# Optimization experiments

Hardware: AMD Instinct MI355X
Metric: run time of the kernel (lower is better)

Reference implementation:

```python
import jax, jax.numpy as jnp
import numpy as np
from jax.scipy.special import erf

B, S, D = 8, 512, 512
H = 8            # num_heads per half
DH = D // 2      # 256, per-branch model dim
DFF = 2048
HOUT = 2


def _layernorm(x, g, b, eps=1e-6):
    mu = jnp.mean(x, axis=-1, keepdims=True)
    var = jnp.mean(jnp.square(x - mu), axis=-1, keepdims=True)
    return (x - mu) / jnp.sqrt(var + eps) * g + b


def _rescale_dist(w):
    one = jnp.float32(1.0)
    return (one + jnp.exp(one)) / (one + jnp.exp(one - w))


def _mha(xin, wq, bq, wk, bk, wv, bv, wo, bo, maskf, adjoin, dist):
    b, s, dm = xin.shape
    dep = dm // H
    def heads(t):
        return t.reshape(b, s, H, dep).transpose(0, 2, 1, 3)  # (b,h,s,dep)
    q = heads(xin @ wq + bq)
    k = heads(xin @ wk + bk)
    v = heads(xin @ wv + bv)
    scores = jnp.einsum('bhqd,bhkd->bhqk', q, k)
    scale = jnp.sqrt(jnp.float32(dep))
    if dist is not None:
        scores = jax.nn.relu(scores) * _rescale_dist(dist) / scale
    else:
        scores = scores / scale
    scores = scores + maskf * jnp.float32(-1e9)
    if adjoin is not None:
        scores = scores + adjoin
    attn = jax.nn.softmax(scores, axis=-1)
    out = jnp.einsum('bhqk,bhkd->bhqd', attn, v).transpose(0, 2, 1, 3).reshape(b, s, dm)
    return out @ wo + bo, attn


def setup_inputs() -> dict:
    key = jax.random.key(0)
    ks = jax.random.split(key, 32)
    init = lambda k, shp: (jax.random.normal(k, shp, dtype=jnp.float32) * 0.02)
    inp = {
        'x': jax.random.normal(ks[0], (B, S, D), dtype=jnp.float32),
        'adjoin_matrix': jax.random.normal(ks[1], (B, 1, S, S), dtype=jnp.float32),
        'dist_matrix': jax.random.uniform(ks[2], (B, 1, S, S), dtype=jnp.float32),
        # mha1 (adjoin branch)
        'wq1': init(ks[3], (DH, DH)), 'bq1': jnp.zeros((DH,), jnp.float32),
        'wk1': init(ks[4], (DH, DH)), 'bk1': jnp.zeros((DH,), jnp.float32),
        'wv1': init(ks[5], (DH, DH)), 'bv1': jnp.zeros((DH,), jnp.float32),
        'wo1': init(ks[6], (DH, DH)), 'bo1': jnp.zeros((DH,), jnp.float32),
        # mha2 (distance branch)
        'wq2': init(ks[7], (DH, DH)), 'bq2': jnp.zeros((DH,), jnp.float32),
        'wk2': init(ks[8], (DH, DH)), 'bk2': jnp.zeros((DH,), jnp.float32),
        'wv2': init(ks[9], (DH, DH)), 'bv2': jnp.zeros((DH,), jnp.float32),
        'wo2': init(ks[10], (DH, DH)), 'bo2': jnp.zeros((DH,), jnp.float32),
        # BANLayer
        'vnet_w': init(ks[11], (DH, 2 * DH)), 'vnet_b': jnp.zeros((2 * DH,), jnp.float32),
        'qnet_w': init(ks[12], (DH, 2 * DH)), 'qnet_b': jnp.zeros((2 * DH,), jnp.float32),
        'h_mat': init(ks[13], (1, HOUT, 1, 2 * DH)),
        'h_bias': init(ks[14], (1, HOUT, 1, 1)),
        'bn_gamma': jnp.ones((D,), jnp.float32), 'bn_beta': jnp.zeros((D,), jnp.float32),
        'bn_mean': jnp.zeros((D,), jnp.float32), 'bn_var': jnp.ones((D,), jnp.float32),
        # LayerNorms
        'ln1_g': jnp.ones((D,), jnp.float32), 'ln1_b': jnp.zeros((D,), jnp.float32),
        'ln2_g': jnp.ones((D,), jnp.float32), 'ln2_b': jnp.zeros((D,), jnp.float32),
        # FFN
        'ffn_w1': init(ks[15], (D, DFF)), 'ffn_b1': jnp.zeros((DFF,), jnp.float32),
        'ffn_w2': init(ks[16], (DFF, D)), 'ffn_b2': jnp.zeros((D,), jnp.float32),
        # padding mask (int -> cast), 1 = masked
        'encoder_padding_mask': jax.random.randint(ks[17], (B, 1, 1, S), 0, 2, dtype=jnp.int32),
    }
    return inp


def reference(x, adjoin_matrix, dist_matrix,
              wq1, bq1, wk1, bk1, wv1, bv1, wo1, bo1,
              wq2, bq2, wk2, bk2, wv2, bv2, wo2, bo2,
              vnet_w, vnet_b, qnet_w, qnet_b, h_mat, h_bias,
              bn_gamma, bn_beta, bn_mean, bn_var,
              ln1_g, ln1_b, ln2_g, ln2_b,
              ffn_w1, ffn_b1, ffn_w2, ffn_b2,
              encoder_padding_mask):
    maskf = encoder_padding_mask.astype(jnp.float32)
    x1, x2 = jnp.split(x, 2, axis=-1)
    # local branch: adjoin bias, no distance
    x_l, aw_local = _mha(x1, wq1, bq1, wk1, bk1, wv1, bv1, wo1, bo1, maskf, adjoin_matrix, None)
    # global branch: relu + distance rescale, no adjoin
    x_g, aw_global = _mha(x2, wq2, bq2, wk2, bk2, wv2, bv2, wo2, bo2, maskf, None, dist_matrix)
    # BANLayer (h_out=2 <= c, eval mode; p_net is identity for rows=1)
    v_ = jax.nn.relu(x_l @ vnet_w + vnet_b)   # (B,S,2*DH)
    q_ = jax.nn.relu(x_g @ qnet_w + qnet_b)
    att_maps = jnp.einsum('xhyk,bvk,bqk->bhvq', h_mat, v_, q_) + h_bias  # (B,HOUT,S,S)
    logits = jnp.einsum('bvk,bhvq,bqk->bvk', v_, att_maps, q_)           # sum over h
    logits = (logits - bn_mean) / jnp.sqrt(bn_var + 1e-3) * bn_gamma + bn_beta
    attn_output = logits * jnp.concatenate([x_l, x_g], axis=-1)
    out1 = _layernorm(x + attn_output, ln1_g, ln1_b)
    h = out1 @ ffn_w1 + ffn_b1
    h = 0.5 * h * (1.0 + erf(h / jnp.sqrt(jnp.float32(2.0))))  # exact gelu
    ffn_out = h @ ffn_w2 + ffn_b2
    out2 = _layernorm(out1 + ffn_out, ln2_g, ln2_b)
    return (out2, aw_local, aw_global)
```

## Files before the change

### kernel.cpp

```cpp
#include <hip/hip_runtime.h>
#include <hip/hip_bf16.h>

typedef __hip_bfloat16 bf16;
typedef __attribute__((ext_vector_type(8))) short bf16x8;
typedef __attribute__((ext_vector_type(4))) float f32x4;

#define BB 8
#define SS 512
#define DD 512
#define NH 8
#define DHm 256
#define DFF 2048

__device__ __forceinline__ void gl_lds16(const void* g, void* l) {
  __builtin_amdgcn_global_load_lds((const __attribute__((address_space(1))) void*)g,
                                   (__attribute__((address_space(3))) void*)l, 16, 0, 0);
}

__device__ __forceinline__ bf16x8 cvt8(const float* p) {
  union { bf16x8 v; bf16 h[8]; } u;
  float4 f0 = *(const float4*)p, f1 = *(const float4*)(p + 4);
  u.h[0]=__float2bfloat16(f0.x); u.h[1]=__float2bfloat16(f0.y);
  u.h[2]=__float2bfloat16(f0.z); u.h[3]=__float2bfloat16(f0.w);
  u.h[4]=__float2bfloat16(f1.x); u.h[5]=__float2bfloat16(f1.y);
  u.h[6]=__float2bfloat16(f1.z); u.h[7]=__float2bfloat16(f1.w);
  return u.v;
}

template<int BM, int BN, int SMODE, int BIASM, int ACT>
__global__ __launch_bounds__(256)
void gemm2(const bf16* __restrict__ A, const bf16* __restrict__ B,
           const float* __restrict__ bias, float* __restrict__ Cf,
           bf16* __restrict__ Cb, int K, int lda, int ldb, int ldc,
           long long sA, long long sB, long long sC)
{
  __shared__ bf16 As[BM * 32];
  __shared__ bf16 Bs[BN * 32];
  const int t = threadIdx.x, lane = t & 63, wave = t >> 6;
  const int l15 = lane & 15, quad = lane >> 4;
  constexpr int WMT = BM / 32, WNT = BN / 32;
  const int wm = (wave & 1) * (BM / 2), wn = (wave >> 1) * (BN / 2);
  const int row0 = blockIdx.y * BM, col0 = blockIdx.x * BN;
  const bf16* Ab = A + (long long)blockIdx.z * sA + (long long)row0 * lda;
  const bf16* Bb = B + (long long)blockIdx.z * sB + (long long)col0 * ldb;
  const int srow = wave * 16 + (lane >> 2), skc = (lane & 3) << 3;

  f32x4 acc[WMT][WNT] = {};

  for (int k0 = 0; k0 < K; k0 += 32) {
#pragma unroll
    for (int j = 0; j < BM / 64; j++)
      gl_lds16(Ab + (long long)(srow + j * 64) * lda + k0 + skc,
               (char*)As + wave * 1024 + j * 4096);
#pragma unroll
    for (int j = 0; j < BN / 64; j++)
      gl_lds16(Bb + (long long)(srow + j * 64) * ldb + k0 + skc,
               (char*)Bs + wave * 1024 + j * 4096);
    __syncthreads();
    bf16x8 af[WMT], bfr[WNT];
#pragma unroll
    for (int i = 0; i < WMT; i++) af[i]  = *(const bf16x8*)&As[(wm + i * 16 + l15) * 32 + quad * 8];
#pragma unroll
    for (int j = 0; j < WNT; j++) bfr[j] = *(const bf16x8*)&Bs[(wn + j * 16 + l15) * 32 + quad * 8];
#pragma unroll
    for (int i = 0; i < WMT; i++)
#pragma unroll
      for (int j = 0; j < WNT; j++)
        acc[i][j] = __builtin_amdgcn_mfma_f32_16x16x32_bf16(af[i], bfr[j], acc[i][j], 0, 0, 0);
    __syncthreads();
  }

  float sb = 0.f;
  if (BIASM == 2) sb = bias[0] + bias[1];
#pragma unroll
  for (int i = 0; i < WMT; i++)
#pragma unroll
    for (int j = 0; j < WNT; j++) {
      int col = col0 + wn + j * 16 + l15;
      float bv = (BIASM == 1) ? bias[col] : sb;
#pragma unroll
      for (int r = 0; r < 4; r++) {
        int row = row0 + wm + i * 16 + (quad << 2) + r;
        float v = acc[i][j][r] + bv;
        if (ACT == 1) v = fmaxf(v, 0.f);
        if (ACT == 2) v = 0.5f * v * (1.f + erff(v * 0.70710678118654752f));
        long long ci = (long long)blockIdx.z * sC + (long long)row * ldc + col;
        if (SMODE & 1) Cf[ci] = v;
        if (SMODE & 2) Cb[ci] = __float2bfloat16(v);
      }
    }
}

template<int BRANCH>
__global__ __launch_bounds__(256, 2)
void attn_mfma(const bf16* __restrict__ QKV, const int* __restrict__ mask,
               const float* __restrict__ extra, float* __restrict__ aw,
               bf16* __restrict__ ctx)
{
  const int qt = blockIdx.x, h = blockIdx.y, b = blockIdx.z;
  const int t = threadIdx.x, lane = t & 63, wave = t >> 6;
  const int l15 = lane & 15, quad = lane >> 4;
  __shared__ bf16x8 Vt[64][32];

  {
    const bf16* Vb = QKV + (long long)b * SS * 768 + 512 + h * 32;
    int dep = t & 31;
#pragma unroll
    for (int j8 = 0; j8 < 8; j8++) {
      int blk = (t >> 5) + (j8 << 3);
      union { bf16x8 v; bf16 hh[8]; } u;
#pragma unroll
      for (int i = 0; i < 8; i++)
        u.hh[i] = Vb[(long long)(blk * 8 + i) * 768 + dep];
      Vt[blk][dep] = u.v;
    }
  }

  const int q0 = qt * 64 + wave * 16;
  const bf16* Qb = QKV + ((long long)(b * SS + q0)) * 768 + h * 32;
  bf16x8 qfrag = *(const bf16x8*)(Qb + (long long)l15 * 768 + quad * 8);
  __syncthreads();

  const float scale_inv = 0.17677669529663688f;
  const bf16* Kb = QKV + (long long)b * SS * 768 + 256 + h * 32;
  const float* Eb = extra + ((long long)b * SS + q0) * SS;
  float sreg[32][4];
  float rmax[4] = {-1e30f, -1e30f, -1e30f, -1e30f};
#pragma unroll
  for (int kc = 0; kc < 32; kc++) {
    int kpos = kc * 16 + l15;
    bf16x8 kfrag = *(const bf16x8*)(Kb + (long long)kpos * 768 + quad * 8);
    f32x4 a = __builtin_amdgcn_mfma_f32_16x16x32_bf16(qfrag, kfrag, f32x4{0.f,0.f,0.f,0.f}, 0, 0, 0);
    float mval = (float)mask[b * SS + kpos] * -1e9f;
#pragma unroll
    for (int r = 0; r < 4; r++) {
      float s = a[r];
      float ev = Eb[(long long)(quad * 4 + r) * SS + kpos];
      if (BRANCH == 1) {
        s = s * scale_inv + mval + ev;
      } else {
        float resc = 3.7182818284590452f / (1.f + __expf(1.f - ev));
        s = fmaxf(s, 0.f) * resc * scale_inv + mval;
      }
      sreg[kc][r] = s;
      rmax[r] = fmaxf(rmax[r], s);
    }
  }
#pragma unroll
  for (int r = 0; r < 4; r++) {
    float v = rmax[r];
    v = fmaxf(v, __shfl_xor(v, 1, 16));
    v = fmaxf(v, __shfl_xor(v, 2, 16));
    v = fmaxf(v, __shfl_xor(v, 4, 16));
    v = fmaxf(v, __shfl_xor(v, 8, 16));
    rmax[r] = v;
  }
  float rsum[4] = {0.f, 0.f, 0.f, 0.f};
#pragma unroll
  for (int kc = 0; kc < 32; kc++)
#pragma unroll
    for (int r = 0; r < 4; r++) {
      float e = __expf(sreg[kc][r] - rmax[r]);
      sreg[kc][r] = e;
      rsum[r] += e;
    }
#pragma unroll
  for (int r = 0; r < 4; r++) {
    float v = rsum[r];
    v += __shfl_xor(v, 1, 16);
    v += __shfl_xor(v, 2, 16);
    v += __shfl_xor(v, 4, 16);
    v += __shfl_xor(v, 8, 16);
    rsum[r] = 1.f / v;
  }
  float* awp = aw + (((long long)(b * NH + h) * SS + q0)) * SS;
#pragma unroll
  for (int kc = 0; kc < 32; kc++)
#pragma unroll
    for (int r = 0; r < 4; r++)
      awp[(long long)(quad * 4 + r) * SS + kc * 16 + l15] = sreg[kc][r] * rsum[r];

  asm volatile("s_waitcnt vmcnt(0)" ::: "memory");

  f32x4 oacc[2] = {};
#pragma unroll
  for (int kc2 = 0; kc2 < 16; kc2++) {
    bf16x8 afr = cvt8(awp + (long long)l15 * SS + kc2 * 32 + quad * 8);
#pragma unroll
    for (int n = 0; n < 2; n++) {
      bf16x8 bfr = Vt[kc2 * 4 + quad][n * 16 + l15];
      oacc[n] = __builtin_amdgcn_mfma_f32_16x16x32_bf16(afr, bfr, oacc[n], 0, 0, 0);
    }
  }
#pragma unroll
  for (int n = 0; n < 2; n++)
#pragma unroll
    for (int r = 0; r < 4; r++) {
      int q = q0 + quad * 4 + r;
      ctx[(long long)(b * SS + q) * DHm + h * 32 + n * 16 + l15] = __float2bfloat16(oacc[n][r]);
    }
}

__device__ __forceinline__ void tr_tile(const float* __restrict__ src, bf16* __restrict__ dst,
                                        int K, int N, int tile) {
  __shared__ float tl[32][33];
  int tilesN = N >> 5;
  int tk = tile / tilesN, tn = tile % tilesN;
  int c = threadIdx.x & 31, r0 = threadIdx.x >> 5;
#pragma unroll
  for (int i = 0; i < 4; i++) {
    int r = r0 + i * 8;
    tl[r][c] = src[(long long)(tk * 32 + r) * N + tn * 32 + c];
  }
  __syncthreads();
#pragma unroll
  for (int i = 0; i < 4; i++) {
    int r = r0 + i * 8;
    dst[(long long)(tn * 32 + r) * K + tk * 32 + c] = __float2bfloat16(tl[c][r]);
  }
}

__global__ __launch_bounds__(256)
void pack_all(const float* wq1, const float* wk1, const float* wv1,
              const float* wq2, const float* wk2, const float* wv2,
              const float* wo1, const float* wo2,
              const float* vnet_w, const float* qnet_w,
              const float* ffn_w1, const float* ffn_w2,
              const float* bq1, const float* bk1, const float* bv1,
              const float* bq2, const float* bk2, const float* bv2,
              const float* x,
              bf16* WB1, bf16* WB2, bf16* woT1, bf16* woT2,
              bf16* vnetT, bf16* qnetT, bf16* f1T, bf16* f2T,
              float* BB1v, float* BB2v, bf16* xb)
{
  int blk = blockIdx.x;
  if (blk < 64)        { tr_tile(wq1, WB1,            256, 256, blk); return; }
  if (blk < 128)       { tr_tile(wk1, WB1 + 256*256,  256, 256, blk-64); return; }
  if (blk < 192)       { tr_tile(wv1, WB1 + 512*256,  256, 256, blk-128); return; }
  if (blk < 256)       { tr_tile(wq2, WB2,            256, 256, blk-192); return; }
  if (blk < 320)       { tr_tile(wk2, WB2 + 256*256,  256, 256, blk-256); return; }
  if (blk < 384)       { tr_tile(wv2, WB2 + 512*256,  256, 256, blk-320); return; }
  if (blk < 448)       { tr_tile(wo1, woT1,           256, 256, blk-384); return; }
  if (blk < 512)       { tr_tile(wo2, woT2,           256, 256, blk-448); return; }
  if (blk < 640)       { tr_tile(vnet_w, vnetT,       256, 512, blk-512); return; }
  if (blk < 768)       { tr_tile(qnet_w, qnetT,       256, 512, blk-640); return; }
  if (blk < 1792)      { tr_tile(ffn_w1, f1T,         512, 2048, blk-768); return; }
  if (blk < 2816)      { tr_tile(ffn_w2, f2T,         2048, 512, blk-1792); return; }
  if (blk < 3840) {
    long long i0 = (long long)(blk - 2816) * 2048 + threadIdx.x * 8;
    *(bf16x8*)(xb + i0) = cvt8(x + i0);
    return;
  }
  {
    int b = blk - 3840;
    const float* src = b==0?bq1 : b==1?bk1 : b==2?bv1 : b==3?bq2 : b==4?bk2 : bv2;
    float* dst = (b < 3 ? BB1v : BB2v) + (b % 3) * 256;
    dst[threadIdx.x] = src[threadIdx.x];
  }
}

__global__ __launch_bounds__(256)
void tr_qn(const bf16* __restrict__ Qn, bf16* __restrict__ QnT)
{
  int b = blockIdx.z, tk = blockIdx.y, tn = blockIdx.x;
  __shared__ bf16 tl[32][33];
  int c = threadIdx.x & 31, r0 = threadIdx.x >> 5;
  const bf16* src = Qn + (long long)b * 512 * 512;
  bf16* dst = QnT + (long long)b * 512 * 512;
#pragma unroll
  for (int i = 0; i < 4; i++) { int r = r0 + i * 8; tl[r][c] = src[(tk * 32 + r) * 512 + tn * 32 + c]; }
  __syncthreads();
#pragma unroll
  for (int i = 0; i < 4; i++) { int r = r0 + i * 8; dst[(tn * 32 + r) * 512 + tk * 32 + c] = tl[c][r]; }
}

__global__ __launch_bounds__(256)
void vh_kernel(const bf16* __restrict__ v_, const float* __restrict__ hmat,
               bf16* __restrict__ vh, int n)
{
  int i = blockIdx.x * 256 + threadIdx.x;
  if (i < n) {
    int c = i & (DD - 1);
    vh[i] = __float2bfloat16(__bfloat162float(v_[i]) * (hmat[c] + hmat[DD + c]));
  }
}

__global__ __launch_bounds__(256)
void bn_gate_ln1_kernel(const float* __restrict__ x, const bf16* __restrict__ vbuf,
                        const float* __restrict__ T, const float* __restrict__ xl,
                        const float* __restrict__ xg,
                        const float* __restrict__ bng, const float* __restrict__ bnb,
                        const float* __restrict__ bnm, const float* __restrict__ bnv,
                        const float* __restrict__ lng, const float* __restrict__ lnb,
                        float* __restrict__ out1, bf16* __restrict__ out1b)
{
  const int row = blockIdx.x;
  const int t = threadIdx.x;
  __shared__ float red[256];
  float val[2];
#pragma unroll
  for (int i = 0; i < 2; i++) {
    int c = t + i * 256;
    long long idx = (long long)row * DD + c;
    float lg = __bfloat162float(vbuf[idx]) * T[idx];
    float bn = (lg - bnm[c]) / sqrtf(bnv[c] + 1e-3f) * bng[c] + bnb[c];
    float gate = (c < DHm) ? xl[(long long)row * DHm + c] : xg[(long long)row * DHm + (c - DHm)];
    val[i] = x[idx] + bn * gate;
  }
  red[t] = val[0] + val[1];
  __syncthreads();
  for (int o = 128; o > 0; o >>= 1) { if (t < o) red[t] += red[t + o]; __syncthreads(); }
  float mu = red[0] * (1.f / 512.f);
  __syncthreads();
  float d0 = val[0] - mu, d1 = val[1] - mu;
  red[t] = d0 * d0 + d1 * d1;
  __syncthreads();
  for (int o = 128; o > 0; o >>= 1) { if (t < o) red[t] += red[t + o]; __syncthreads(); }
  float inv = 1.f / sqrtf(red[0] * (1.f / 512.f) + 1e-6f);
  float o0 = d0 * inv * lng[t] + lnb[t];
  float o1 = d1 * inv * lng[t + 256] + lnb[t + 256];
  out1[(long long)row * DD + t] = o0;
  out1[(long long)row * DD + t + 256] = o1;
  out1b[(long long)row * DD + t] = __float2bfloat16(o0);
  out1b[(long long)row * DD + t + 256] = __float2bfloat16(o1);
}

__global__ __launch_bounds__(256)
void ln2_kernel(const float* __restrict__ a, const float* __restrict__ b2,
                const float* __restrict__ g, const float* __restrict__ bta,
                float* __restrict__ out)
{
  const int row = blockIdx.x;
  const int t = threadIdx.x;
  __shared__ float red[256];
  float v0 = a[(long long)row * DD + t]       + b2[(long long)row * DD + t];
  float v1 = a[(long long)row * DD + t + 256] + b2[(long long)row * DD + t + 256];
  red[t] = v0 + v1;
  __syncthreads();
  for (int o = 128; o > 0; o >>= 1) { if (t < o) red[t] += red[t + o]; __syncthreads(); }
  float mu = red[0] * (1.f / 512.f);
  __syncthreads();
  float d0 = v0 - mu, d1 = v1 - mu;
  red[t] = d0 * d0 + d1 * d1;
  __syncthreads();
  for (int o = 128; o > 0; o >>= 1) { if (t < o) red[t] += red[t + o]; __syncthreads(); }
  float inv = 1.f / sqrtf(red[0] * (1.f / 512.f) + 1e-6f);
  out[(long long)row * DD + t]       = d0 * inv * g[t]       + bta[t];
  out[(long long)row * DD + t + 256] = d1 * inv * g[t + 256] + bta[t + 256];
}

extern "C" void kernel_launch(void* const* d_in, const int* in_sizes, int n_in,
                              void* d_out, int out_size, void* d_ws, size_t ws_size,
                              hipStream_t stream) {
  const float* x      = (const float*)d_in[0];
  const float* adjoin = (const float*)d_in[1];
  const float* dist   = (const float*)d_in[2];
  const float* wq1=(const float*)d_in[3],  *bq1=(const float*)d_in[4];
  const float* wk1=(const float*)d_in[5],  *bk1=(const float*)d_in[6];
  const float* wv1=(const float*)d_in[7],  *bv1=(const float*)d_in[8];
  const float* wo1=(const float*)d_in[9],  *bo1=(const float*)d_in[10];
  const float* wq2=(const float*)d_in[11], *bq2=(const float*)d_in[12];
  const float* wk2=(const float*)d_in[13], *bk2=(const float*)d_in[14];
  const float* wv2=(const float*)d_in[15], *bv2=(const float*)d_in[16];
  const float* wo2=(const float*)d_in[17], *bo2=(const float*)d_in[18];
  const float* vnet_w=(const float*)d_in[19], *vnet_b=(const float*)d_in[20];
  const float* qnet_w=(const float*)d_in[21], *qnet_b=(const float*)d_in[22];
  const float* h_mat=(const float*)d_in[23], *h_bias=(const float*)d_in[24];
  const float* bn_g=(const float*)d_in[25], *bn_b=(const float*)d_in[26];
  const float* bn_m=(const float*)d_in[27], *bn_v=(const float*)d_in[28];
  const float* ln1_g=(const float*)d_in[29], *ln1_b=(const float*)d_in[30];
  const float* ln2_g=(const float*)d_in[31], *ln2_b=(const float*)d_in[32];
  const float* ffn_w1=(const float*)d_in[33], *ffn_b1=(const float*)d_in[34];
  const float* ffn_w2=(const float*)d_in[35], *ffn_b2=(const float*)d_in[36];
  const int* mask = (const int*)d_in[37];

  char* base = (char*)d_ws;
  size_t off = 0;
  auto alloc = [&](size_t bytes) { char* p = base + off; off += (bytes + 255) & ~(size_t)255; return p; };
  bf16*  xb    = (bf16*) alloc(4096LL*512*2);
  bf16*  WB1   = (bf16*) alloc(768*256*2);
  bf16*  WB2   = (bf16*) alloc(768*256*2);
  float* BB1v  = (float*)alloc(768*4);
  float* BB2v  = (float*)alloc(768*4);
  bf16*  woT1  = (bf16*) alloc(256*256*2);
  bf16*  woT2  = (bf16*) alloc(256*256*2);
  bf16*  vnetT = (bf16*) alloc(512*256*2);
  bf16*  qnetT = (bf16*) alloc(512*256*2);
  bf16*  f1T   = (bf16*) alloc(2048*512*2);
  bf16*  f2T   = (bf16*) alloc(512*2048*2);
  bf16*  QKV1  = (bf16*) alloc(4096LL*768*2);
  bf16*  QKV2  = (bf16*) alloc(4096LL*768*2);
  bf16*  CTX   = (bf16*) alloc(4096LL*256*2);
  float* XL    = (float*)alloc(4096LL*256*4);
  float* XG    = (float*)alloc(4096LL*256*4);
  bf16*  XLb   = (bf16*) alloc(4096LL*256*2);
  bf16*  XGb   = (bf16*) alloc(4096LL*256*2);
  bf16*  Vn    = (bf16*) alloc(4096LL*512*2);
  bf16*  Qn    = (bf16*) alloc(4096LL*512*2);
  bf16*  QnT   = (bf16*) alloc(4096LL*512*2);
  bf16*  VH    = (bf16*) alloc(4096LL*512*2);
  bf16*  G     = (bf16*) alloc(8LL*512*512*2);
  float* T     = (float*)alloc(4096LL*512*4);
  float* OUT1  = (float*)alloc(4096LL*512*4);
  bf16*  OUT1b = (bf16*) alloc(4096LL*512*2);
  bf16*  H     = (bf16*) alloc(4096LL*2048*2);
  float* FFNO  = (float*)alloc(4096LL*512*4);

  float* out2 = (float*)d_out;
  float* awl  = out2 + 2097152LL;
  float* awg  = awl + 16777216LL;

  const int MR = BB * SS;
  const long long GST = (long long)SS * SS;

  pack_all<<<dim3(3846), 256, 0, stream>>>(
      wq1, wk1, wv1, wq2, wk2, wv2, wo1, wo2, vnet_w, qnet_w, ffn_w1, ffn_w2,
      bq1, bk1, bv1, bq2, bk2, bv2, x,
      WB1, WB2, woT1, woT2, vnetT, qnetT, f1T, f2T, BB1v, BB2v, xb);

  gemm2<128,128,2,1,0><<<dim3(6, 32, 1), 256, 0, stream>>>(
      xb,       WB1, BB1v, nullptr, QKV1, 256, 512, 256, 768, 0, 0, 0);
  gemm2<128,128,2,1,0><<<dim3(6, 32, 1), 256, 0, stream>>>(
      xb + 256, WB2, BB2v, nullptr, QKV2, 256, 512, 256, 768, 0, 0, 0);

  attn_mfma<1><<<dim3(8, NH, BB), 256, 0, stream>>>(QKV1, mask, adjoin, awl, CTX);
  gemm2<64,64,3,1,0><<<dim3(4, 64, 1), 256, 0, stream>>>(
      CTX, woT1, bo1, XL, XLb, 256, 256, 256, 256, 0, 0, 0);
  attn_mfma<2><<<dim3(8, NH, BB), 256, 0, stream>>>(QKV2, mask, dist, awg, CTX);
  gemm2<64,64,3,1,0><<<dim3(4, 64, 1), 256, 0, stream>>>(
      CTX, woT2, bo2, XG, XGb, 256, 256, 256, 256, 0, 0, 0);

  gemm2<64,64,2,1,1><<<dim3(8, 64, 1), 256, 0, stream>>>(
      XLb, vnetT, vnet_b, nullptr, Vn, 256, 256, 256, 512, 0, 0, 0);
  gemm2<64,64,2,1,1><<<dim3(8, 64, 1), 256, 0, stream>>>(
      XGb, qnetT, qnet_b, nullptr, Qn, 256, 256, 256, 512, 0, 0, 0);
  vh_kernel<<<dim3((MR * DD) / 256), 256, 0, stream>>>(Vn, h_mat, VH, MR * DD);
  tr_qn<<<dim3(16, 16, BB), 256, 0, stream>>>(Qn, QnT);
  gemm2<64,64,2,2,0><<<dim3(8, 8, BB), 256, 0, stream>>>(
      VH, Qn, h_bias, nullptr, G, 512, 512, 512, 512, GST, GST, GST);
  gemm2<64,64,1,0,0><<<dim3(8, 8, BB), 256, 0, stream>>>(
      G, QnT, nullptr, T, nullptr, 512, 512, 512, 512, GST, GST, GST);

  bn_gate_ln1_kernel<<<dim3(MR), 256, 0, stream>>>(
      x, Vn, T, XL, XG, bn_g, bn_b, bn_m, bn_v, ln1_g, ln1_b, OUT1, OUT1b);

  gemm2<128,128,2,1,2><<<dim3(16, 32, 1), 256, 0, stream>>>(
      OUT1b, f1T, ffn_b1, nullptr, H, 512, 512, 512, 2048, 0, 0, 0);
  gemm2<64,64,1,1,0><<<dim3(8, 64, 1), 256, 0, stream>>>(
      H, f2T, ffn_b2, FFNO, nullptr, 2048, 2048, 2048, 512, 0, 0, 0);

  ln2_kernel<<<dim3(MR), 256, 0, stream>>>(OUT1, FFNO, ln2_g, ln2_b, out2);
}
```

Measured before the change: 451.1 us.

## Batch both branches per launch, fuse VH/transposes into epilogues, widen GEMM K-step

Both attention branches, their QKV and output projections, and the vnet/qnet projections now run as single launches, using blockIdx.z to pick the branch. The vnet/qnet GEMM epilogue writes the h_mat-scaled V and the transposed Q directly, which removes the separate vh and transpose kernels. The GEMM loads a K=64 tile per stage into XOR-swizzled LDS to cut bank conflicts and halve the barrier count. Several intermediates (T, FFN output, gated branch outputs) are stored in bf16 instead of fp32, which cuts memory traffic but lowers precision.

```diff
diff --git a/kernel.cpp b/kernel.cpp
--- a/kernel.cpp
+++ b/kernel.cpp
@@ -27,46 +27,58 @@
   return u.v;
 }
 
-template<int BM, int BN, int SMODE, int BIASM, int ACT>
+template<int BM, int BN, int SMODE, int BIASM, int ACT, int EXTRA>
 __global__ __launch_bounds__(256)
 void gemm2(const bf16* __restrict__ A, const bf16* __restrict__ B,
            const float* __restrict__ bias, float* __restrict__ Cf,
            bf16* __restrict__ Cb, int K, int lda, int ldb, int ldc,
-           long long sA, long long sB, long long sC)
+           long long sA, long long sB, long long sC, long long sBias,
+           const float* __restrict__ hs, bf16* __restrict__ E0, bf16* __restrict__ E1)
 {
-  __shared__ bf16 As[BM * 32];
-  __shared__ bf16 Bs[BN * 32];
+  __shared__ bf16 As[BM * 64];
+  __shared__ bf16 Bs[BN * 64];
   const int t = threadIdx.x, lane = t & 63, wave = t >> 6;
   const int l15 = lane & 15, quad = lane >> 4;
   constexpr int WMT = BM / 32, WNT = BN / 32;
   const int wm = (wave & 1) * (BM / 2), wn = (wave >> 1) * (BN / 2);
+  const int z = blockIdx.z;
   const int row0 = blockIdx.y * BM, col0 = blockIdx.x * BN;
-  const bf16* Ab = A + (long long)blockIdx.z * sA + (long long)row0 * lda;
-  const bf16* Bb = B + (long long)blockIdx.z * sB + (long long)col0 * ldb;
-  const int srow = wave * 16 + (lane >> 2), skc = (lane & 3) << 3;
+  const bf16* Ab = A + (long long)z * sA + (long long)row0 * lda;
+  const bf16* Bb = B + (long long)z * sB + (long long)col0 * ldb;
+  const int srow = wave * 8 + (lane >> 3);
+  const int skc  = (((lane & 7) ^ (lane >> 3)) << 3);
 
   f32x4 acc[WMT][WNT] = {};
 
-  for (int k0 = 0; k0 < K; k0 += 32) {
-#pragma unroll
-    for (int j = 0; j < BM / 64; j++)
-      gl_lds16(Ab + (long long)(srow + j * 64) * lda + k0 + skc,
-               (char*)As + wave * 1024 + j * 4096);
-#pragma unroll
-    for (int j = 0; j < BN / 64; j++)
-      gl_lds16(Bb + (long long)(srow + j * 64) * ldb + k0 + skc,
-               (char*)Bs + wave * 1024 + j * 4096);
+  for (int k0 = 0; k0 < K; k0 += 64) {
+#pragma unroll
+    for (int j = 0; j < BM / 32; j++)
+      gl_lds16(Ab + (long long)(srow + j * 32) * lda + k0 + skc,
+               (char*)As + j * 4096 + wave * 1024);
+#pragma unroll
+    for (int j = 0; j < BN / 32; j++)
+      gl_lds16(Bb + (long long)(srow + j * 32) * ldb + k0 + skc,
+               (char*)Bs + j * 4096 + wave * 1024);
     __syncthreads();
-    bf16x8 af[WMT], bfr[WNT];
-#pragma unroll
-    for (int i = 0; i < WMT; i++) af[i]  = *(const bf16x8*)&As[(wm + i * 16 + l15) * 32 + quad * 8];
-#pragma unroll
-    for (int j = 0; j < WNT; j++) bfr[j] = *(const bf16x8*)&Bs[(wn + j * 16 + l15) * 32 + quad * 8];
-#pragma unroll
-    for (int i = 0; i < WMT; i++)
-#pragma unroll
-      for (int j = 0; j < WNT; j++)
-        acc[i][j] = __builtin_amdgcn_mfma_f32_16x16x32_bf16(af[i], bfr[j], acc[i][j], 0, 0, 0);
+#pragma unroll
+    for (int h = 0; h < 2; h++) {
+      bf16x8 af[WMT], bfr[WNT];
+#pragma unroll
+      for (int i = 0; i < WMT; i++) {
+        int m = wm + i * 16 + l15;
+        af[i] = *(const bf16x8*)&As[m * 64 + (((h * 4 + quad) ^ (m & 7)) << 3)];
+      }
+#pragma unroll
+      for (int j = 0; j < WNT; j++) {
+        int n = wn + j * 16 + l15;
+        bfr[j] = *(const bf16x8*)&Bs[n * 64 + (((h * 4 + quad) ^ (n & 7)) << 3)];
+      }
+#pragma unroll
+      for (int i = 0; i < WMT; i++)
+#pragma unroll
+        for (int j = 0; j < WNT; j++)
+          acc[i][j] = __builtin_amdgcn_mfma_f32_16x16x32_bf16(af[i], bfr[j], acc[i][j], 0, 0, 0);
+    }
     __syncthreads();
   }
 
@@ -77,33 +89,43 @@
 #pragma unroll
     for (int j = 0; j < WNT; j++) {
       int col = col0 + wn + j * 16 + l15;
-      float bv = (BIASM == 1) ? bias[col] : sb;
+      float bv = (BIASM == 1) ? bias[(long long)z * sBias + col] : sb;
+      float hv = (EXTRA == 1) ? hs[col] : 0.f;
 #pragma unroll
       for (int r = 0; r < 4; r++) {
         int row = row0 + wm + i * 16 + (quad << 2) + r;
         float v = acc[i][j][r] + bv;
         if (ACT == 1) v = fmaxf(v, 0.f);
         if (ACT == 2) v = 0.5f * v * (1.f + erff(v * 0.70710678118654752f));
-        long long ci = (long long)blockIdx.z * sC + (long long)row * ldc + col;
+        long long ci = (long long)z * sC + (long long)row * ldc + col;
         if (SMODE & 1) Cf[ci] = v;
         if (SMODE & 2) Cb[ci] = __float2bfloat16(v);
+        if (EXTRA == 1) {
+          if (z == 0) E0[(long long)row * ldc + col] = __float2bfloat16(v * hv);
+          else {
+            int bb = row >> 9, q = row & 511;
+            E1[((long long)bb << 18) + (long long)col * 512 + q] = __float2bfloat16(v);
+          }
+        }
       }
     }
 }
 
-template<int BRANCH>
 __global__ __launch_bounds__(256, 2)
 void attn_mfma(const bf16* __restrict__ QKV, const int* __restrict__ mask,
-               const float* __restrict__ extra, float* __restrict__ aw,
+               const float* __restrict__ adjoin, const float* __restrict__ dist,
+               float* __restrict__ awl, float* __restrict__ awg,
                bf16* __restrict__ ctx)
 {
-  const int qt = blockIdx.x, h = blockIdx.y, b = blockIdx.z;
+  const int qt = blockIdx.x, h = blockIdx.y;
+  const int b = blockIdx.z & 7, br = blockIdx.z >> 3;
   const int t = threadIdx.x, lane = t & 63, wave = t >> 6;
   const int l15 = lane & 15, quad = lane >> 4;
   __shared__ bf16x8 Vt[64][32];
 
+  const bf16* QKVb = QKV + (long long)br * 4096 * 768;
   {
-    const bf16* Vb = QKV + (long long)b * SS * 768 + 512 + h * 32;
+    const bf16* Vb = QKVb + (long long)b * SS * 768 + 512 + h * 32;
     int dep = t & 31;
 #pragma unroll
     for (int j8 = 0; j8 < 8; j8++) {
@@ -117,13 +139,13 @@
   }
 
   const int q0 = qt * 64 + wave * 16;
-  const bf16* Qb = QKV + ((long long)(b * SS + q0)) * 768 + h * 32;
+  const bf16* Qb = QKVb + ((long long)(b * SS + q0)) * 768 + h * 32;
   bf16x8 qfrag = *(const bf16x8*)(Qb + (long long)l15 * 768 + quad * 8);
   __syncthreads();
 
   const float scale_inv = 0.17677669529663688f;
-  const bf16* Kb = QKV + (long long)b * SS * 768 + 256 + h * 32;
-  const float* Eb = extra + ((long long)b * SS + q0) * SS;
+  const bf16* Kb = QKVb + (long long)b * SS * 768 + 256 + h * 32;
+  const float* Eb = (br == 0 ? adjoin : dist) + ((long long)b * SS + q0) * SS;
   float sreg[32][4];
   float rmax[4] = {-1e30f, -1e30f, -1e30f, -1e30f};
 #pragma unroll
@@ -136,7 +158,7 @@
     for (int r = 0; r < 4; r++) {
       float s = a[r];
       float ev = Eb[(long long)(quad * 4 + r) * SS + kpos];
-      if (BRANCH == 1) {
+      if (br == 0) {
         s = s * scale_inv + mval + ev;
       } else {
         float resc = 3.7182818284590452f / (1.f + __expf(1.f - ev));
@@ -173,7 +195,7 @@
     v += __shfl_xor(v, 8, 16);
     rsum[r] = 1.f / v;
   }
-  float* awp = aw + (((long long)(b * NH + h) * SS + q0)) * SS;
+  float* awp = (br == 0 ? awl : awg) + (((long long)(b * NH + h) * SS + q0)) * SS;
 #pragma unroll
   for (int kc = 0; kc < 32; kc++)
 #pragma unroll
@@ -192,12 +214,13 @@
       oacc[n] = __builtin_amdgcn_mfma_f32_16x16x32_bf16(afr, bfr, oacc[n], 0, 0, 0);
     }
   }
+  bf16* ctxb = ctx + (long long)br * 4096 * DHm;
 #pragma unroll
   for (int n = 0; n < 2; n++)
 #pragma unroll
     for (int r = 0; r < 4; r++) {
       int q = q0 + quad * 4 + r;
-      ctx[(long long)(b * SS + q) * DHm + h * 32 + n * 16 + l15] = __float2bfloat16(oacc[n][r]);
+      ctxb[(long long)(b * SS + q) * DHm + h * 32 + n * 16 + l15] = __float2bfloat16(oacc[n][r]);
     }
 }
 
@@ -228,12 +251,16 @@
               const float* ffn_w1, const float* ffn_w2,
               const float* bq1, const float* bk1, const float* bv1,
               const float* bq2, const float* bk2, const float* bv2,
+              const float* bo1, const float* bo2,
+              const float* vnet_b, const float* qnet_b, const float* h_mat,
               const float* x,
               bf16* WB1, bf16* WB2, bf16* woT1, bf16* woT2,
               bf16* vnetT, bf16* qnetT, bf16* f1T, bf16* f2T,
-              float* BB1v, float* BB2v, bf16* xb)
+              float* BB1v, float* BB2v, float* BO2, float* BVQ, float* HS,
+              bf16* xb)
 {
   int blk = blockIdx.x;
+  int t = threadIdx.x;
   if (blk < 64)        { tr_tile(wq1, WB1,            256, 256, blk); return; }
   if (blk < 128)       { tr_tile(wk1, WB1 + 256*256,  256, 256, blk-64); return; }
   if (blk < 192)       { tr_tile(wv1, WB1 + 512*256,  256, 256, blk-128); return; }
@@ -247,48 +274,24 @@
   if (blk < 1792)      { tr_tile(ffn_w1, f1T,         512, 2048, blk-768); return; }
   if (blk < 2816)      { tr_tile(ffn_w2, f2T,         2048, 512, blk-1792); return; }
   if (blk < 3840) {
-    long long i0 = (long long)(blk - 2816) * 2048 + threadIdx.x * 8;
+    long long i0 = (long long)(blk - 2816) * 2048 + t * 8;
     *(bf16x8*)(xb + i0) = cvt8(x + i0);
     return;
   }
-  {
-    int b = blk - 3840;
-    const float* src = b==0?bq1 : b==1?bk1 : b==2?bv1 : b==3?bq2 : b==4?bk2 : bv2;
-    float* dst = (b < 3 ? BB1v : BB2v) + (b % 3) * 256;
-    dst[threadIdx.x] = src[threadIdx.x];
-  }
-}
-
-__global__ __launch_bounds__(256)
-void tr_qn(const bf16* __restrict__ Qn, bf16* __restrict__ QnT)
-{
-  int b = blockIdx.z, tk = blockIdx.y, tn = blockIdx.x;
-  __shared__ bf16 tl[32][33];
-  int c = threadIdx.x & 31, r0 = threadIdx.x >> 5;
-  const bf16* src = Qn + (long long)b * 512 * 512;
-  bf16* dst = QnT + (long long)b * 512 * 512;
-#pragma unroll
-  for (int i = 0; i < 4; i++) { int r = r0 + i * 8; tl[r][c] = src[(tk * 32 + r) * 512 + tn * 32 + c]; }
-  __syncthreads();
-#pragma unroll
-  for (int i = 0; i < 4; i++) { int r = r0 + i * 8; dst[(tn * 32 + r) * 512 + tk * 32 + c] = tl[c][r]; }
-}
-
-__global__ __launch_bounds__(256)
-void vh_kernel(const bf16* __restrict__ v_, const float* __restrict__ hmat,
-               bf16* __restrict__ vh, int n)
-{
-  int i = blockIdx.x * 256 + threadIdx.x;
-  if (i < n) {
-    int c = i & (DD - 1);
-    vh[i] = __float2bfloat16(__bfloat162float(v_[i]) * (hmat[c] + hmat[DD + c]));
-  }
+  int i = blk - 3840;
+  if (i < 6) {
+    const float* src = i==0?bq1 : i==1?bk1 : i==2?bv1 : i==3?bq2 : i==4?bk2 : bv2;
+    float* dst = (i < 3 ? BB1v : BB2v) + (i % 3) * 256;
+    dst[t] = src[t];
+  } else if (i < 8)  { BO2[(i-6)*256 + t] = (i==6 ? bo1 : bo2)[t]; }
+  else if (i < 10)   { BVQ[(i-8)*256 + t] = vnet_b[(i-8)*256 + t]; }
+  else if (i < 12)   { BVQ[512 + (i-10)*256 + t] = qnet_b[(i-10)*256 + t]; }
+  else               { int c = (i-12)*256 + t; HS[c] = h_mat[c] + h_mat[512 + c]; }
 }
 
 __global__ __launch_bounds__(256)
 void bn_gate_ln1_kernel(const float* __restrict__ x, const bf16* __restrict__ vbuf,
-                        const float* __restrict__ T, const float* __restrict__ xl,
-                        const float* __restrict__ xg,
+                        const bf16* __restrict__ T, const bf16* __restrict__ xlg,
                         const float* __restrict__ bng, const float* __restrict__ bnb,
                         const float* __restrict__ bnm, const float* __restrict__ bnv,
                         const float* __restrict__ lng, const float* __restrict__ lnb,
@@ -302,9 +305,10 @@
   for (int i = 0; i < 2; i++) {
     int c = t + i * 256;
     long long idx = (long long)row * DD + c;
-    float lg = __bfloat162float(vbuf[idx]) * T[idx];
+    float lg = __bfloat162float(vbuf[idx]) * __bfloat162float(T[idx]);
     float bn = (lg - bnm[c]) / sqrtf(bnv[c] + 1e-3f) * bng[c] + bnb[c];
-    float gate = (c < DHm) ? xl[(long long)row * DHm + c] : xg[(long long)row * DHm + (c - DHm)];
+    long long gidx = (long long)(c >> 8) * 4096 * DHm + (long long)row * DHm + (c & 255);
+    float gate = __bfloat162float(xlg[gidx]);
     val[i] = x[idx] + bn * gate;
   }
   red[t] = val[0] + val[1];
@@ -326,15 +330,15 @@
 }
 
 __global__ __launch_bounds__(256)
-void ln2_kernel(const float* __restrict__ a, const float* __restrict__ b2,
+void ln2_kernel(const float* __restrict__ a, const bf16* __restrict__ b2,
                 const float* __restrict__ g, const float* __restrict__ bta,
                 float* __restrict__ out)
 {
   const int row = blockIdx.x;
   const int t = threadIdx.x;
   __shared__ float red[256];
-  float v0 = a[(long long)row * DD + t]       + b2[(long long)row * DD + t];
-  float v1 = a[(long long)row * DD + t + 256] + b2[(long long)row * DD + t + 256];
+  float v0 = a[(long long)row * DD + t]       + __bfloat162float(b2[(long long)row * DD + t]);
+  float v1 = a[(long long)row * DD + t + 256] + __bfloat162float(b2[(long long)row * DD + t + 256]);
   red[t] = v0 + v1;
   __syncthreads();
   for (int o = 128; o > 0; o >>= 1) { if (t < o) red[t] += red[t + o]; __syncthreads(); }
@@ -388,23 +392,22 @@
   bf16*  qnetT = (bf16*) alloc(512*256*2);
   bf16*  f1T   = (bf16*) alloc(2048*512*2);
   bf16*  f2T   = (bf16*) alloc(512*2048*2);
-  bf16*  QKV1  = (bf16*) alloc(4096LL*768*2);
-  bf16*  QKV2  = (bf16*) alloc(4096LL*768*2);
-  bf16*  CTX   = (bf16*) alloc(4096LL*256*2);
-  float* XL    = (float*)alloc(4096LL*256*4);
-  float* XG    = (float*)alloc(4096LL*256*4);
-  bf16*  XLb   = (bf16*) alloc(4096LL*256*2);
-  bf16*  XGb   = (bf16*) alloc(4096LL*256*2);
+  float* BO2   = (float*)alloc(512*4);
+  float* BVQ   = (float*)alloc(1024*4);
+  float* HS    = (float*)alloc(512*4);
+  bf16*  QKV   = (bf16*) alloc(2LL*4096*768*2);
+  bf16*  CTX   = (bf16*) alloc(2LL*4096*256*2);
+  bf16*  XLG   = (bf16*) alloc(2LL*4096*256*2);
   bf16*  Vn    = (bf16*) alloc(4096LL*512*2);
   bf16*  Qn    = (bf16*) alloc(4096LL*512*2);
   bf16*  QnT   = (bf16*) alloc(4096LL*512*2);
   bf16*  VH    = (bf16*) alloc(4096LL*512*2);
   bf16*  G     = (bf16*) alloc(8LL*512*512*2);
-  float* T     = (float*)alloc(4096LL*512*4);
+  bf16*  T     = (bf16*) alloc(4096LL*512*2);
   float* OUT1  = (float*)alloc(4096LL*512*4);
   bf16*  OUT1b = (bf16*) alloc(4096LL*512*2);
   bf16*  H     = (bf16*) alloc(4096LL*2048*2);
-  float* FFNO  = (float*)alloc(4096LL*512*4);
+  bf16*  FFNO  = (bf16*) alloc(4096LL*512*2);
 
   float* out2 = (float*)d_out;
   float* awl  = out2 + 2097152LL;
@@ -413,41 +416,43 @@
   const int MR = BB * SS;
   const long long GST = (long long)SS * SS;
 
-  pack_all<<<dim3(3846), 256, 0, stream>>>(
+  pack_all<<<dim3(3854), 256, 0, stream>>>(
       wq1, wk1, wv1, wq2, wk2, wv2, wo1, wo2, vnet_w, qnet_w, ffn_w1, ffn_w2,
-      bq1, bk1, bv1, bq2, bk2, bv2, x,
-      WB1, WB2, woT1, woT2, vnetT, qnetT, f1T, f2T, BB1v, BB2v, xb);
-
-  gemm2<128,128,2,1,0><<<dim3(6, 32, 1), 256, 0, stream>>>(
-      xb,       WB1, BB1v, nullptr, QKV1, 256, 512, 256, 768, 0, 0, 0);
-  gemm2<128,128,2,1,0><<<dim3(6, 32, 1), 256, 0, stream>>>(
-      xb + 256, WB2, BB2v, nullptr, QKV2, 256, 512, 256, 768, 0, 0, 0);
-
-  attn_mfma<1><<<dim3(8, NH, BB), 256, 0, stream>>>(QKV1, mask, adjoin, awl, CTX);
-  gemm2<64,64,3,1,0><<<dim3(4, 64, 1), 256, 0, stream>>>(
-      CTX, woT1, bo1, XL, XLb, 256, 256, 256, 256, 0, 0, 0);
-  attn_mfma<2><<<dim3(8, NH, BB), 256, 0, stream>>>(QKV2, mask, dist, awg, CTX);
-  gemm2<64,64,3,1,0><<<dim3(4, 64, 1), 256, 0, stream>>>(
-      CTX, woT2, bo2, XG, XGb, 256, 256, 256, 256, 0, 0, 0);
-
-  gemm2<64,64,2,1,1><<<dim3(8, 64, 1), 256, 0, stream>>>(
-      XLb, vnetT, vnet_b, nullptr, Vn, 256, 256, 256, 512, 0, 0, 0);
-  gemm2<64,64,2,1,1><<<dim3(8, 64, 1), 256, 0, stream>>>(
-      XGb, qnetT, qnet_b, nullptr, Qn, 256, 256, 256, 512, 0, 0, 0);
-  vh_kernel<<<dim3((MR * DD) / 256), 256, 0, stream>>>(Vn, h_mat, VH, MR * DD);
-  tr_qn<<<dim3(16, 16, BB), 256, 0, stream>>>(Qn, QnT);
-  gemm2<64,64,2,2,0><<<dim3(8, 8, BB), 256, 0, stream>>>(
-      VH, Qn, h_bias, nullptr, G, 512, 512, 512, 512, GST, GST, GST);
-  gemm2<64,64,1,0,0><<<dim3(8, 8, BB), 256, 0, stream>>>(
-      G, QnT, nullptr, T, nullptr, 512, 512, 512, 512, GST, GST, GST);
+      bq1, bk1, bv1, bq2, bk2, bv2, bo1, bo2, vnet_b, qnet_b, h_mat, x,
+      WB1, WB2, woT1, woT2, vnetT, qnetT, f1T, f2T, BB1v, BB2v, BO2, BVQ, HS, xb);
+
+  gemm2<128,64,2,1,0,0><<<dim3(768/64, MR/128, 2), 256, 0, stream>>>(
+      xb, WB1, BB1v, nullptr, QKV, 256, 512, 256, 768,
+      256, 768*256, 4096LL*768, 768, nullptr, nullptr, nullptr);
+
+  attn_mfma<<<dim3(8, NH, 16), 256, 0, stream>>>(QKV, mask, adjoin, dist, awl, awg, CTX);
+
+  gemm2<64,64,2,1,0,0><<<dim3(4, 64, 2), 256, 0, stream>>>(
+      CTX, woT1, BO2, nullptr, XLG, 256, 256, 256, 256,
+      4096LL*256, 256*256, 4096LL*256, 256, nullptr, nullptr, nullptr);
+
+  gemm2<64,64,2,1,1,1><<<dim3(8, 64, 2), 256, 0, stream>>>(
+      XLG, vnetT, BVQ, nullptr, Vn, 256, 256, 256, 512,
+      4096LL*256, 512*256, 4096LL*512, 512, HS, VH, QnT);
+
+  gemm2<64,64,2,2,0,0><<<dim3(8, 8, 8), 256, 0, stream>>>(
+      VH, Qn, h_bias, nullptr, G, 512, 512, 512, 512,
+      GST, GST, GST, 0, nullptr, nullptr, nullptr);
+
+  gemm2<64,64,2,0,0,0><<<dim3(8, 8, 8), 256, 0, stream>>>(
+      G, QnT, nullptr, nullptr, T, 512, 512, 512, 512,
+      GST, GST, GST, 0, nullptr, nullptr, nullptr);
 
   bn_gate_ln1_kernel<<<dim3(MR), 256, 0, stream>>>(
-      x, Vn, T, XL, XG, bn_g, bn_b, bn_m, bn_v, ln1_g, ln1_b, OUT1, OUT1b);
-
-  gemm2<128,128,2,1,2><<<dim3(16, 32, 1), 256, 0, stream>>>(
-      OUT1b, f1T, ffn_b1, nullptr, H, 512, 512, 512, 2048, 0, 0, 0);
-  gemm2<64,64,1,1,0><<<dim3(8, 64, 1), 256, 0, stream>>>(
-      H, f2T, ffn_b2, FFNO, nullptr, 2048, 2048, 2048, 512, 0, 0, 0);
+      x, Vn, T, XLG, bn_g, bn_b, bn_m, bn_v, ln1_g, ln1_b, OUT1, OUT1b);
+
+  gemm2<128,128,2,1,2,0><<<dim3(16, 32, 1), 256, 0, stream>>>(
+      OUT1b, f1T, ffn_b1, nullptr, H, 512, 512, 512, 2048,
+      0, 0, 0, 0, nullptr, nullptr, nullptr);
+
+  gemm2<64,64,2,1,0,0><<<dim3(8, 64, 1), 256, 0, stream>>>(
+      H, f2T, ffn_b2, nullptr, FFNO, 2048, 2048, 2048, 512,
+      0, 0, 0, 0, nullptr, nullptr, nullptr);
 
   ln2_kernel<<<dim3(MR), 256, 0, stream>>>(OUT1, FFNO, ln2_g, ln2_b, out2);
 }
```

Result: slower. 479.3 us (+6.3%).
